# Kernel optimization log

Hardware: AMD Instinct MI355X
Metric: run time of the kernel (lower is better)

The kernel has to match this reference:

```python
import jax, jax.numpy as jnp
import numpy as np

B, T, S, C, F = 32, 50, 2048, 8, 32  # batch, time, spatial steps, in-channels, filters
K, STRIDE = 2, 2
DN = ('NWC', 'WIO', 'NWC')


def hard_sigmoid(x):
    # TF-Keras hard_sigmoid: clip(0.2*x + 0.5, 0, 1)
    return jnp.clip(0.2 * x + 0.5, 0.0, 1.0)


def setup_inputs() -> dict:
    key = jax.random.key(0)
    ks = jax.random.split(key, 5)
    x = jax.random.normal(ks[0], (B, T, S, C), jnp.float32)
    kernel = jax.random.normal(ks[1], (K, C, 4 * F), jnp.float32) * 0.05
    rec_kernel = jax.random.normal(ks[2], (K, F, 4 * F), jnp.float32) * 0.05
    bias = jnp.zeros((4 * F,), jnp.float32)
    dense_w = jax.random.normal(ks[3], ((S // STRIDE) * F, 1), jnp.float32) * 0.02
    dense_b = jnp.zeros((1,), jnp.float32)
    return dict(x=x, kernel=kernel, rec_kernel=rec_kernel, bias=bias,
                dense_w=dense_w, dense_b=dense_b)


def reference(x, kernel, rec_kernel, bias, dense_w, dense_b):
    b, t, s, c = x.shape
    f = rec_kernel.shape[1]
    # Input convolution for all timesteps at once (stride 2, SAME padding)
    xc = jax.lax.conv_general_dilated(x.reshape(b * t, s, c), kernel,
                                      (STRIDE,), 'SAME', dimension_numbers=DN)
    xc = xc + bias
    sh = xc.shape[1]  # ceil(s / stride)
    xc = xc.reshape(b, t, sh, 4 * f).transpose(1, 0, 2, 3)  # time-major for scan

    def step(carry, xt):
        h, cst = carry
        hc = jax.lax.conv_general_dilated(h, rec_kernel, (1,), 'SAME',
                                          dimension_numbers=DN)
        z = xt + hc
        zi, zf, zc, zo = jnp.split(z, 4, axis=-1)
        i = hard_sigmoid(zi)
        fg = hard_sigmoid(zf)
        cst = fg * cst + i * jnp.tanh(zc)
        o = hard_sigmoid(zo)
        h = o * jnp.tanh(cst)
        return (h, cst), None

    h0 = jnp.zeros((b, sh, f), x.dtype)
    (h, _), _ = jax.lax.scan(step, (h0, h0), xc)
    # Flatten + Dense(1)
    return h.reshape(b, -1) @ dense_w + dense_b
```

## Files before the change

kernel.cpp:

```cpp
#include <hip/hip_runtime.h>


#define TT 50
#define LTILE 64
#define ROWS 129
#define HSTR 40

typedef __attribute__((ext_vector_type(8))) short short8;
typedef __attribute__((ext_vector_type(4))) float floatx4;

__device__ short8 g_tw0[512];
__device__ short8 g_tw1[512];
__device__ short8 g_txw[512];

__device__ __forceinline__ unsigned short f2b_rne(float f) {
  union { float f; unsigned u; } v; v.f = f;
  unsigned r = v.u + 0x7FFFu + ((v.u >> 16) & 1u);
  return (unsigned short)(r >> 16);
}
__device__ __forceinline__ unsigned short f2b_trunc(float f) {
  union { float f; unsigned u; } v; v.f = f;
  return (unsigned short)(v.u >> 16);
}
__device__ __forceinline__ float hsig(float x) {
  return __builtin_amdgcn_fmed3f(__builtin_fmaf(0.2f, x, 0.5f), 0.0f, 1.0f);
}
__device__ __forceinline__ float ftanh(float x) {
  float e = __expf(2.0f * x);
  return 1.0f - 2.0f * __builtin_amdgcn_rcpf(e + 1.0f);
}

__global__ void prep(const float* __restrict__ ks,
                     const float* __restrict__ rks,
                     const float* __restrict__ bs,
                     float* __restrict__ ws) {
  const int lane = threadIdx.x;
  if (lane < 32) ws[lane] = 0.0f;
  const int q  = lane >> 4;
  const int f0 = lane & 15;
#pragma unroll
  for (int n = 0; n < 8; ++n) {
    const int oc = (n >> 1) * 32 + 2 * f0 + (n & 1);
    short8 th;
#pragma unroll
    for (int j = 0; j < 8; ++j)
      th[j] = (short)f2b_rne(rks[(q * 8 + j) * 128 + oc]);
    g_tw0[n * 64 + lane] = th;
#pragma unroll
    for (int j = 0; j < 8; ++j)
      th[j] = (short)f2b_rne(rks[(32 + q * 8 + j) * 128 + oc]);
    g_tw1[n * 64 + lane] = th;
    short8 tx = {0, 0, 0, 0, 0, 0, 0, 0};
    if (q < 2) {
#pragma unroll
      for (int j = 0; j < 8; ++j)
        tx[j] = (short)f2b_rne(ks[(q * 8 + j) * 128 + oc]);
    } else if (q == 2) {
      tx[0] = (short)f2b_rne(bs[oc]);
    }
    g_txw[n * 64 + lane] = tx;
  }
}

__global__ __launch_bounds__(256, 2)
void convlstm_scan(const float* __restrict__ xs,
                   const float* __restrict__ dws,
                   float* __restrict__ acc_out) {
  __shared__ short hbH[2][ROWS * HSTR];

  const int tid  = threadIdx.x;
  const int b    = blockIdx.x >> 4;
  const int j0   = (blockIdx.x & 15) * LTILE;
  const int wave = tid >> 6;
  const int lane = tid & 63;
  const int q    = lane >> 4;
  const int f0   = lane & 15;

  for (int e = tid; e < ROWS * HSTR; e += 256)
    ((int*)hbH)[e] = 0;

  short8 Bwh0[8], Bwh1[8], Bxw[8];
#pragma unroll
  for (int n = 0; n < 8; ++n) {
    Bwh0[n] = g_tw0[n * 64 + lane];
    Bwh1[n] = g_tw1[n * 64 + lane];
    Bxw[n]  = g_txw[n * 64 + lane];
  }

  short8 axc = {0, 0, 0, 0, 0, 0, 0, 0};
  if (q == 2) axc[0] = (short)0x3F80;

  const floatx4 zero4 = {0.0f, 0.0f, 0.0f, 0.0f};

  float cst[2][8];
#pragma unroll
  for (int s = 0; s < 2; ++s)
#pragma unroll
    for (int i = 0; i < 8; ++i) cst[s][i] = 0.0f;

  floatx4 px0[2], px1[2];
#pragma unroll
  for (int s = 0; s < 2; ++s) {
    const int jr = (wave + 4 * s) * 16 + f0;
    const int jm = min(j0 + jr, 1023);
    const float* xp = xs + (size_t)b * TT * (2048 * 8) +
                      (size_t)(2 * jm + (q & 1)) * 8;
    px0[s] = *(const floatx4*)xp;
    px1[s] = *(const floatx4*)(xp + 4);
  }

  const int maxrows = 1024 - j0;
  float part = 0.0f;
  __syncthreads();

  for (int t = 0; t < TT; ++t) {
    const short* curH = hbH[t & 1];
    short* nxtH = hbH[(t & 1) ^ 1];
    int rows = LTILE + (TT - 1) - t;
    if (rows > maxrows) rows = maxrows;
    const int nmt = (rows + 15) >> 4;
    const int act1 = (wave + 4) < nmt;
    const int last = (t == TT - 1);
    const int tn = last ? t : t + 1;
    const float* xnext = xs + ((size_t)(b * TT + tn)) * (2048 * 8);

    short8 a0h[2], a1h[2];
#pragma unroll
    for (int s = 0; s < 2; ++s) {
      const int jr = (wave + 4 * s) * 16 + f0;
      a0h[s] = *(const short8*)&curH[jr * HSTR + q * 8];
      a1h[s] = *(const short8*)&curH[(jr + 1) * HSTR + q * 8];
    }

    short8 ax[2];
#pragma unroll
    for (int s = 0; s < 2; ++s) {
      ax[s] = axc;
      if (q < 2) {
        floatx4 x0 = px0[s], x1 = px1[s];
#pragma unroll
        for (int jj = 0; jj < 4; ++jj) ax[s][jj] = (short)f2b_trunc(x0[jj]);
#pragma unroll
        for (int jj = 0; jj < 4; ++jj) ax[s][4 + jj] = (short)f2b_trunc(x1[jj]);
      }
    }

#pragma unroll
    for (int s = 0; s < 2; ++s) {
      const int jr = (wave + 4 * s) * 16 + f0;
      const int jm = min(j0 + jr, 1023);
      const float* xp = xnext + (size_t)(2 * jm + (q & 1)) * 8;
      px0[s] = *(const floatx4*)xp;
      px1[s] = *(const floatx4*)(xp + 4);
    }

#pragma unroll
    for (int s = 0; s < 2; ++s) {
      if (s == 1 && !act1) continue;
      const int m = wave + 4 * s;

      floatx4 acc[8];
#pragma unroll
      for (int n = 0; n < 8; ++n)
        acc[n] = __builtin_amdgcn_mfma_f32_16x16x32_bf16(ax[s], Bxw[n], zero4, 0, 0, 0);
#pragma unroll
      for (int n = 0; n < 8; ++n)
        acc[n] = __builtin_amdgcn_mfma_f32_16x16x32_bf16(a0h[s], Bwh0[n], acc[n], 0, 0, 0);
#pragma unroll
      for (int n = 0; n < 8; ++n)
        acc[n] = __builtin_amdgcn_mfma_f32_16x16x32_bf16(a1h[s], Bwh1[n], acc[n], 0, 0, 0);

      const int jw = m * 16 + q * 4;
#pragma unroll
      for (int r = 0; r < 4; ++r) {
        float hv2[2];
#pragma unroll
        for (int p = 0; p < 2; ++p) {
          float zi = acc[0 + p][r], zf = acc[2 + p][r];
          float zc = acc[4 + p][r], zo = acc[6 + p][r];
          float ig = hsig(zi), fg = hsig(zf), og = hsig(zo);
          float cs = cst[s][p * 4 + r];
          float cn = __builtin_fmaf(fg, cs, ig * ftanh(zc));
          cst[s][p * 4 + r] = cn;
          hv2[p] = og * ftanh(cn);
        }
        if (!last) {
          unsigned pk;
          asm("v_cvt_pk_bf16_f32 %0, %1, %2"
              : "=v"(pk) : "v"(hv2[0]), "v"(hv2[1]));
          *(unsigned*)&nxtH[(jw + r) * HSTR + 2 * f0] = pk;
        } else {
          const int di = (j0 + jw + r) * 32 + 2 * f0;
          part = __builtin_fmaf(hv2[0], dws[di],
                 __builtin_fmaf(hv2[1], dws[di + 1], part));
        }
      }
    }
    __syncthreads();
  }

#pragma unroll
  for (int off = 32; off > 0; off >>= 1) part += __shfl_down(part, off);
  if (lane == 0) atomicAdd(&acc_out[b], part);
}

__global__ void finalize(const float* __restrict__ ws,
                         const float* __restrict__ db,
                         float* __restrict__ out) {
  int i = threadIdx.x;
  if (i < 32) out[i] = ws[i] + db[0];
}

extern "C" void kernel_launch(void* const* d_in, const int* in_sizes, int n_in,
                              void* d_out, int out_size, void* d_ws, size_t ws_size,
                              hipStream_t stream) {
  const float* x  = (const float*)d_in[0];
  const float* k  = (const float*)d_in[1];
  const float* rk = (const float*)d_in[2];
  const float* bi = (const float*)d_in[3];
  const float* dw = (const float*)d_in[4];
  const float* db = (const float*)d_in[5];
  float* ws = (float*)d_ws;
  float* out = (float*)d_out;

  hipLaunchKernelGGL(prep, dim3(1), dim3(64), 0, stream, k, rk, bi, ws);
  hipLaunchKernelGGL(convlstm_scan, dim3(512), dim3(256), 0, stream,
                     x, dw, ws);
  hipLaunchKernelGGL(finalize, dim3(1), dim3(64), 0, stream, ws, db, out);
}
```

Measured before the change: 233.4 us.

## Assign one M-tile per wave with 512-thread blocks and skip idle waves

The scan kernel doubles its block to 8 waves, so each wave owns a single 16-row tile instead of looping over two. The per-wave cell state and x-prefetch registers shrink, and waves whose tile falls outside the shrinking active row range skip all work for that step. The partial-sum atomic is limited to the first four waves, since only they hold rows at the final step. The launch bound of (512, 4) caps registers per thread tightly. With about 96 VGPRs already used for resident bf16 weight fragments, this risks spills, and each block-wide barrier now spans more waves.

```diff
diff --git a/kernel.cpp b/kernel.cpp
--- a/kernel.cpp
+++ b/kernel.cpp
@@ -62,7 +62,7 @@
   }
 }
 
-__global__ __launch_bounds__(256, 2)
+__global__ __launch_bounds__(512, 4)
 void convlstm_scan(const float* __restrict__ xs,
                    const float* __restrict__ dws,
                    float* __restrict__ acc_out) {
@@ -76,7 +76,7 @@
   const int q    = lane >> 4;
   const int f0   = lane & 15;
 
-  for (int e = tid; e < ROWS * HSTR; e += 256)
+  for (int e = tid; e < ROWS * HSTR; e += 512)
     ((int*)hbH)[e] = 0;
 
   short8 Bwh0[8], Bwh1[8], Bxw[8];
@@ -92,21 +92,18 @@
 
   const floatx4 zero4 = {0.0f, 0.0f, 0.0f, 0.0f};
 
-  float cst[2][8];
-#pragma unroll
-  for (int s = 0; s < 2; ++s)
-#pragma unroll
-    for (int i = 0; i < 8; ++i) cst[s][i] = 0.0f;
-
-  floatx4 px0[2], px1[2];
-#pragma unroll
-  for (int s = 0; s < 2; ++s) {
-    const int jr = (wave + 4 * s) * 16 + f0;
-    const int jm = min(j0 + jr, 1023);
-    const float* xp = xs + (size_t)b * TT * (2048 * 8) +
-                      (size_t)(2 * jm + (q & 1)) * 8;
-    px0[s] = *(const floatx4*)xp;
-    px1[s] = *(const floatx4*)(xp + 4);
+  float cst[8];
+#pragma unroll
+  for (int i = 0; i < 8; ++i) cst[i] = 0.0f;
+
+  const int jr = wave * 16 + f0;
+  const int jm = min(j0 + jr, 1023);
+  const float* xbase = xs + (size_t)b * TT * (2048 * 8);
+  floatx4 px0 = zero4, px1 = zero4;
+  if (q < 2) {
+    const float* xp = xbase + (size_t)(2 * jm + q) * 8;
+    px0 = *(const floatx4*)xp;
+    px1 = *(const floatx4*)(xp + 4);
   }
 
   const int maxrows = 1024 - j0;
@@ -119,58 +116,39 @@
     int rows = LTILE + (TT - 1) - t;
     if (rows > maxrows) rows = maxrows;
     const int nmt = (rows + 15) >> 4;
-    const int act1 = (wave + 4) < nmt;
     const int last = (t == TT - 1);
-    const int tn = last ? t : t + 1;
-    const float* xnext = xs + ((size_t)(b * TT + tn)) * (2048 * 8);
-
-    short8 a0h[2], a1h[2];
-#pragma unroll
-    for (int s = 0; s < 2; ++s) {
-      const int jr = (wave + 4 * s) * 16 + f0;
-      a0h[s] = *(const short8*)&curH[jr * HSTR + q * 8];
-      a1h[s] = *(const short8*)&curH[(jr + 1) * HSTR + q * 8];
-    }
-
-    short8 ax[2];
-#pragma unroll
-    for (int s = 0; s < 2; ++s) {
-      ax[s] = axc;
+
+    if (wave < nmt) {
+      short8 a0h = *(const short8*)&curH[jr * HSTR + q * 8];
+      short8 a1h = *(const short8*)&curH[(jr + 1) * HSTR + q * 8];
+
+      short8 ax = axc;
       if (q < 2) {
-        floatx4 x0 = px0[s], x1 = px1[s];
-#pragma unroll
-        for (int jj = 0; jj < 4; ++jj) ax[s][jj] = (short)f2b_trunc(x0[jj]);
-#pragma unroll
-        for (int jj = 0; jj < 4; ++jj) ax[s][4 + jj] = (short)f2b_trunc(x1[jj]);
+#pragma unroll
+        for (int jj = 0; jj < 4; ++jj) ax[jj] = (short)f2b_trunc(px0[jj]);
+#pragma unroll
+        for (int jj = 0; jj < 4; ++jj) ax[4 + jj] = (short)f2b_trunc(px1[jj]);
       }
-    }
-
-#pragma unroll
-    for (int s = 0; s < 2; ++s) {
-      const int jr = (wave + 4 * s) * 16 + f0;
-      const int jm = min(j0 + jr, 1023);
-      const float* xp = xnext + (size_t)(2 * jm + (q & 1)) * 8;
-      px0[s] = *(const floatx4*)xp;
-      px1[s] = *(const floatx4*)(xp + 4);
-    }
-
-#pragma unroll
-    for (int s = 0; s < 2; ++s) {
-      if (s == 1 && !act1) continue;
-      const int m = wave + 4 * s;
+
+      const int tn = last ? t : t + 1;
+      if (q < 2) {
+        const float* xp = xbase + ((size_t)tn * 2048 + (size_t)(2 * jm + q)) * 8;
+        px0 = *(const floatx4*)xp;
+        px1 = *(const floatx4*)(xp + 4);
+      }
 
       floatx4 acc[8];
 #pragma unroll
       for (int n = 0; n < 8; ++n)
-        acc[n] = __builtin_amdgcn_mfma_f32_16x16x32_bf16(ax[s], Bxw[n], zero4, 0, 0, 0);
+        acc[n] = __builtin_amdgcn_mfma_f32_16x16x32_bf16(ax, Bxw[n], zero4, 0, 0, 0);
 #pragma unroll
       for (int n = 0; n < 8; ++n)
-        acc[n] = __builtin_amdgcn_mfma_f32_16x16x32_bf16(a0h[s], Bwh0[n], acc[n], 0, 0, 0);
+        acc[n] = __builtin_amdgcn_mfma_f32_16x16x32_bf16(a0h, Bwh0[n], acc[n], 0, 0, 0);
 #pragma unroll
       for (int n = 0; n < 8; ++n)
-        acc[n] = __builtin_amdgcn_mfma_f32_16x16x32_bf16(a1h[s], Bwh1[n], acc[n], 0, 0, 0);
-
-      const int jw = m * 16 + q * 4;
+        acc[n] = __builtin_amdgcn_mfma_f32_16x16x32_bf16(a1h, Bwh1[n], acc[n], 0, 0, 0);
+
+      const int jw = wave * 16 + q * 4;
 #pragma unroll
       for (int r = 0; r < 4; ++r) {
         float hv2[2];
@@ -179,9 +157,9 @@
           float zi = acc[0 + p][r], zf = acc[2 + p][r];
           float zc = acc[4 + p][r], zo = acc[6 + p][r];
           float ig = hsig(zi), fg = hsig(zf), og = hsig(zo);
-          float cs = cst[s][p * 4 + r];
+          float cs = cst[p * 4 + r];
           float cn = __builtin_fmaf(fg, cs, ig * ftanh(zc));
-          cst[s][p * 4 + r] = cn;
+          cst[p * 4 + r] = cn;
           hv2[p] = og * ftanh(cn);
         }
         if (!last) {
@@ -201,7 +179,7 @@
 
 #pragma unroll
   for (int off = 32; off > 0; off >>= 1) part += __shfl_down(part, off);
-  if (lane == 0) atomicAdd(&acc_out[b], part);
+  if (lane == 0 && wave < 4) atomicAdd(&acc_out[b], part);
 }
 
 __global__ void finalize(const float* __restrict__ ws,
@@ -224,7 +202,7 @@
   float* out = (float*)d_out;
 
   hipLaunchKernelGGL(prep, dim3(1), dim3(64), 0, stream, k, rk, bi, ws);
-  hipLaunchKernelGGL(convlstm_scan, dim3(512), dim3(256), 0, stream,
+  hipLaunchKernelGGL(convlstm_scan, dim3(512), dim3(512), 0, stream,
                      x, dw, ws);
   hipLaunchKernelGGL(finalize, dim3(1), dim3(64), 0, stream, ws, db, out);
 }
```

Result: slower. 355.0 us (+52.1%).

## Stage MFMA weight fragments in LDS and raise occupancy to three blocks

Applied to the files above, without the earlier changes.

Moves the three sets of bf16 weight fragments out of per-thread registers into shared memory. Each MFMA now reads its B operand from LDS inside the timestep loop, and the launch bound rises to three blocks per CU to exploit the freed VGPRs. Input prefetch is also restricted to the lanes that use it (q<2), which removes redundant global loads. The cost is roughly 24 KB of extra LDS reads per wave per timestep and higher LDS pressure. More resident blocks are meant to hide the latency of the serial scan.

```diff
diff --git a/kernel.cpp b/kernel.cpp
--- a/kernel.cpp
+++ b/kernel.cpp
@@ -62,11 +62,14 @@
   }
 }
 
-__global__ __launch_bounds__(256, 2)
+__global__ __launch_bounds__(256, 3)
 void convlstm_scan(const float* __restrict__ xs,
                    const float* __restrict__ dws,
                    float* __restrict__ acc_out) {
   __shared__ short hbH[2][ROWS * HSTR];
+  __shared__ short8 sTw0[512];
+  __shared__ short8 sTw1[512];
+  __shared__ short8 sTxw[512];
 
   const int tid  = threadIdx.x;
   const int b    = blockIdx.x >> 4;
@@ -78,13 +81,10 @@
 
   for (int e = tid; e < ROWS * HSTR; e += 256)
     ((int*)hbH)[e] = 0;
-
-  short8 Bwh0[8], Bwh1[8], Bxw[8];
-#pragma unroll
-  for (int n = 0; n < 8; ++n) {
-    Bwh0[n] = g_tw0[n * 64 + lane];
-    Bwh1[n] = g_tw1[n * 64 + lane];
-    Bxw[n]  = g_txw[n * 64 + lane];
+  for (int e = tid; e < 512; e += 256) {
+    sTw0[e] = g_tw0[e];
+    sTw1[e] = g_tw1[e];
+    sTxw[e] = g_txw[e];
   }
 
   short8 axc = {0, 0, 0, 0, 0, 0, 0, 0};
@@ -101,12 +101,15 @@
   floatx4 px0[2], px1[2];
 #pragma unroll
   for (int s = 0; s < 2; ++s) {
+    px0[s] = zero4; px1[s] = zero4;
     const int jr = (wave + 4 * s) * 16 + f0;
     const int jm = min(j0 + jr, 1023);
-    const float* xp = xs + (size_t)b * TT * (2048 * 8) +
-                      (size_t)(2 * jm + (q & 1)) * 8;
-    px0[s] = *(const floatx4*)xp;
-    px1[s] = *(const floatx4*)(xp + 4);
+    if (q < 2) {
+      const float* xp = xs + (size_t)b * TT * (2048 * 8) +
+                        (size_t)(2 * jm + q) * 8;
+      px0[s] = *(const floatx4*)xp;
+      px1[s] = *(const floatx4*)(xp + 4);
+    }
   }
 
   const int maxrows = 1024 - j0;
@@ -149,9 +152,11 @@
     for (int s = 0; s < 2; ++s) {
       const int jr = (wave + 4 * s) * 16 + f0;
       const int jm = min(j0 + jr, 1023);
-      const float* xp = xnext + (size_t)(2 * jm + (q & 1)) * 8;
-      px0[s] = *(const floatx4*)xp;
-      px1[s] = *(const floatx4*)(xp + 4);
+      if (q < 2) {
+        const float* xp = xnext + (size_t)(2 * jm + q) * 8;
+        px0[s] = *(const floatx4*)xp;
+        px1[s] = *(const floatx4*)(xp + 4);
+      }
     }
 
 #pragma unroll
@@ -161,14 +166,20 @@
 
       floatx4 acc[8];
 #pragma unroll
-      for (int n = 0; n < 8; ++n)
-        acc[n] = __builtin_amdgcn_mfma_f32_16x16x32_bf16(ax[s], Bxw[n], zero4, 0, 0, 0);
-#pragma unroll
-      for (int n = 0; n < 8; ++n)
-        acc[n] = __builtin_amdgcn_mfma_f32_16x16x32_bf16(a0h[s], Bwh0[n], acc[n], 0, 0, 0);
-#pragma unroll
-      for (int n = 0; n < 8; ++n)
-        acc[n] = __builtin_amdgcn_mfma_f32_16x16x32_bf16(a1h[s], Bwh1[n], acc[n], 0, 0, 0);
+      for (int n = 0; n < 8; ++n) {
+        short8 bx = sTxw[n * 64 + lane];
+        acc[n] = __builtin_amdgcn_mfma_f32_16x16x32_bf16(ax[s], bx, zero4, 0, 0, 0);
+      }
+#pragma unroll
+      for (int n = 0; n < 8; ++n) {
+        short8 bw = sTw0[n * 64 + lane];
+        acc[n] = __builtin_amdgcn_mfma_f32_16x16x32_bf16(a0h[s], bw, acc[n], 0, 0, 0);
+      }
+#pragma unroll
+      for (int n = 0; n < 8; ++n) {
+        short8 bw = sTw1[n * 64 + lane];
+        acc[n] = __builtin_amdgcn_mfma_f32_16x16x32_bf16(a1h[s], bw, acc[n], 0, 0, 0);
+      }
 
       const int jw = m * 16 + q * 4;
 #pragma unroll
```

New measurement: 244.2 us. 4.6% more time.

## Halve recompute halo by exchanging mid-scan boundary state between neighbor tiles

Applied to the files above, without the earlier changes.

Each block used to recompute a halo of 49 extra rows so that it could run all 50 timesteps independently. Now the halo covers only 25 steps. At t=25 each block publishes its h and c boundary state to global memory and raises a flag, and its neighbor spins on that flag and loads the state to extend its tile for the remaining steps. Blocks are assigned in reverse tile order so that producers are scheduled first. Smaller changes also parallelize prep over 512 threads and skip unneeded x loads and inactive LDS reads. The inter-block spin-wait cuts redundant MFMA work, but it depends on co-residency and forward progress and adds a global-memory synchronization point.

```diff
diff --git a/kernel.cpp b/kernel.cpp
--- a/kernel.cpp
+++ b/kernel.cpp
@@ -2,8 +2,9 @@
 
 
 #define TT 50
+#define HD 25
 #define LTILE 64
-#define ROWS 129
+#define ROWS 97
 #define HSTR 40
 
 typedef __attribute__((ext_vector_type(8))) short short8;
@@ -12,6 +13,10 @@
 __device__ short8 g_tw0[512];
 __device__ short8 g_tw1[512];
 __device__ short8 g_txw[512];
+
+__device__ unsigned g_xh[512 * 400];
+__device__ float    g_xc[512 * 800];
+__device__ int      g_flag[512];
 
 __device__ __forceinline__ unsigned short f2b_rne(float f) {
   union { float f; unsigned u; } v; v.f = f;
@@ -34,32 +39,33 @@
                      const float* __restrict__ rks,
                      const float* __restrict__ bs,
                      float* __restrict__ ws) {
-  const int lane = threadIdx.x;
-  if (lane < 32) ws[lane] = 0.0f;
-  const int q  = lane >> 4;
-  const int f0 = lane & 15;
-#pragma unroll
-  for (int n = 0; n < 8; ++n) {
-    const int oc = (n >> 1) * 32 + 2 * f0 + (n & 1);
-    short8 th;
+  const int tid  = threadIdx.x;
+  const int n    = tid >> 6;
+  const int lane = tid & 63;
+  const int q    = lane >> 4;
+  const int f0   = lane & 15;
+  if (tid < 32) ws[tid] = 0.0f;
+  g_flag[tid] = 0;
+
+  const int oc = (n >> 1) * 32 + 2 * f0 + (n & 1);
+  short8 th;
+#pragma unroll
+  for (int j = 0; j < 8; ++j)
+    th[j] = (short)f2b_rne(rks[(q * 8 + j) * 128 + oc]);
+  g_tw0[n * 64 + lane] = th;
+#pragma unroll
+  for (int j = 0; j < 8; ++j)
+    th[j] = (short)f2b_rne(rks[(32 + q * 8 + j) * 128 + oc]);
+  g_tw1[n * 64 + lane] = th;
+  short8 tx = {0, 0, 0, 0, 0, 0, 0, 0};
+  if (q < 2) {
 #pragma unroll
     for (int j = 0; j < 8; ++j)
-      th[j] = (short)f2b_rne(rks[(q * 8 + j) * 128 + oc]);
-    g_tw0[n * 64 + lane] = th;
-#pragma unroll
-    for (int j = 0; j < 8; ++j)
-      th[j] = (short)f2b_rne(rks[(32 + q * 8 + j) * 128 + oc]);
-    g_tw1[n * 64 + lane] = th;
-    short8 tx = {0, 0, 0, 0, 0, 0, 0, 0};
-    if (q < 2) {
-#pragma unroll
-      for (int j = 0; j < 8; ++j)
-        tx[j] = (short)f2b_rne(ks[(q * 8 + j) * 128 + oc]);
-    } else if (q == 2) {
-      tx[0] = (short)f2b_rne(bs[oc]);
-    }
-    g_txw[n * 64 + lane] = tx;
+      tx[j] = (short)f2b_rne(ks[(q * 8 + j) * 128 + oc]);
+  } else if (q == 2) {
+    tx[0] = (short)f2b_rne(bs[oc]);
   }
+  g_txw[n * 64 + lane] = tx;
 }
 
 __global__ __launch_bounds__(256, 2)
@@ -70,11 +76,15 @@
 
   const int tid  = threadIdx.x;
   const int b    = blockIdx.x >> 4;
-  const int j0   = (blockIdx.x & 15) * LTILE;
+  const int pi   = blockIdx.x & 15;
+  const int tj   = 15 - pi;
+  const int j0   = tj << 6;
   const int wave = tid >> 6;
   const int lane = tid & 63;
   const int q    = lane >> 4;
   const int f0   = lane & 15;
+  const bool is_pub = (pi < 15);
+  const bool is_con = (pi >= 1);
 
   for (int e = tid; e < ROWS * HSTR; e += 256)
     ((int*)hbH)[e] = 0;
@@ -89,7 +99,6 @@
 
   short8 axc = {0, 0, 0, 0, 0, 0, 0, 0};
   if (q == 2) axc[0] = (short)0x3F80;
-
   const floatx4 zero4 = {0.0f, 0.0f, 0.0f, 0.0f};
 
   float cst[2][8];
@@ -101,12 +110,15 @@
   floatx4 px0[2], px1[2];
 #pragma unroll
   for (int s = 0; s < 2; ++s) {
+    px0[s] = zero4; px1[s] = zero4;
     const int jr = (wave + 4 * s) * 16 + f0;
     const int jm = min(j0 + jr, 1023);
-    const float* xp = xs + (size_t)b * TT * (2048 * 8) +
-                      (size_t)(2 * jm + (q & 1)) * 8;
-    px0[s] = *(const floatx4*)xp;
-    px1[s] = *(const floatx4*)(xp + 4);
+    if (q < 2) {
+      const float* xp = xs + (size_t)b * TT * (2048 * 8) +
+                        (size_t)(2 * jm + q) * 8;
+      px0[s] = *(const floatx4*)xp;
+      px1[s] = *(const floatx4*)(xp + 4);
+    }
   }
 
   const int maxrows = 1024 - j0;
@@ -114,9 +126,69 @@
   __syncthreads();
 
   for (int t = 0; t < TT; ++t) {
+    if (t == HD) {
+      short* bufH = hbH[HD & 1];
+      if (is_pub) {
+        for (int e = tid; e < 400; e += 256) {
+          const int row = e >> 4, d = e & 15;
+          g_xh[blockIdx.x * 400 + e] = *(const unsigned*)&bufH[row * HSTR + 2 * d];
+        }
+        if (wave == 0) {
+#pragma unroll
+          for (int r = 0; r < 4; ++r)
+#pragma unroll
+            for (int pp = 0; pp < 2; ++pp)
+              g_xc[blockIdx.x * 800 + (q * 4 + r) * 32 + 2 * f0 + pp] = cst[0][pp * 4 + r];
+        } else if (wave == 1) {
+#pragma unroll
+          for (int r = 0; r < 4; ++r)
+            if (q * 4 + r <= 8) {
+#pragma unroll
+              for (int pp = 0; pp < 2; ++pp)
+                g_xc[blockIdx.x * 800 + (16 + q * 4 + r) * 32 + 2 * f0 + pp] = cst[0][pp * 4 + r];
+            }
+        }
+      }
+      __threadfence();
+      __syncthreads();
+      if (is_pub && tid == 0)
+        __hip_atomic_store(&g_flag[blockIdx.x], 1, __ATOMIC_RELEASE,
+                           __HIP_MEMORY_SCOPE_AGENT);
+      if (is_con) {
+        if (tid == 0) {
+          while (__hip_atomic_load(&g_flag[blockIdx.x - 1], __ATOMIC_RELAXED,
+                                   __HIP_MEMORY_SCOPE_AGENT) == 0)
+            __builtin_amdgcn_s_sleep(2);
+        }
+        __syncthreads();
+        __builtin_amdgcn_fence(__ATOMIC_ACQUIRE, "agent");
+        for (int e = tid; e < 400; e += 256) {
+          const int row = e >> 4, d = e & 15;
+          *(unsigned*)&bufH[(64 + row) * HSTR + 2 * d] =
+              g_xh[(blockIdx.x - 1) * 400 + e];
+        }
+        if (wave == 0) {
+#pragma unroll
+          for (int r = 0; r < 4; ++r)
+#pragma unroll
+            for (int pp = 0; pp < 2; ++pp)
+              cst[1][pp * 4 + r] = g_xc[(blockIdx.x - 1) * 800 + (q * 4 + r) * 32 + 2 * f0 + pp];
+        } else if (wave == 1) {
+#pragma unroll
+          for (int r = 0; r < 4; ++r)
+            if (q * 4 + r <= 8) {
+#pragma unroll
+              for (int pp = 0; pp < 2; ++pp)
+                cst[1][pp * 4 + r] = g_xc[(blockIdx.x - 1) * 800 + (16 + q * 4 + r) * 32 + 2 * f0 + pp];
+            }
+        }
+      }
+      __syncthreads();
+    }
+
     const short* curH = hbH[t & 1];
     short* nxtH = hbH[(t & 1) ^ 1];
-    int rows = LTILE + (TT - 1) - t;
+    int rows = LTILE - 1 + ((t < HD) ? HD : TT) - t;
     if (rows > maxrows) rows = maxrows;
     const int nmt = (rows + 15) >> 4;
     const int act1 = (wave + 4) < nmt;
@@ -127,6 +199,7 @@
     short8 a0h[2], a1h[2];
 #pragma unroll
     for (int s = 0; s < 2; ++s) {
+      if (s == 1 && !act1) continue;
       const int jr = (wave + 4 * s) * 16 + f0;
       a0h[s] = *(const short8*)&curH[jr * HSTR + q * 8];
       a1h[s] = *(const short8*)&curH[(jr + 1) * HSTR + q * 8];
@@ -147,9 +220,10 @@
 
 #pragma unroll
     for (int s = 0; s < 2; ++s) {
+      if (q >= 2) continue;
       const int jr = (wave + 4 * s) * 16 + f0;
       const int jm = min(j0 + jr, 1023);
-      const float* xp = xnext + (size_t)(2 * jm + (q & 1)) * 8;
+      const float* xp = xnext + (size_t)(2 * jm + q) * 8;
       px0[s] = *(const floatx4*)xp;
       px1[s] = *(const floatx4*)(xp + 4);
     }
@@ -223,7 +297,7 @@
   float* ws = (float*)d_ws;
   float* out = (float*)d_out;
 
-  hipLaunchKernelGGL(prep, dim3(1), dim3(64), 0, stream, k, rk, bi, ws);
+  hipLaunchKernelGGL(prep, dim3(1), dim3(512), 0, stream, k, rk, bi, ws);
   hipLaunchKernelGGL(convlstm_scan, dim3(512), dim3(256), 0, stream,
                      x, dw, ws);
   hipLaunchKernelGGL(finalize, dim3(1), dim3(64), 0, stream, ws, db, out);
```

Measured after the change: 334.8 us. 43.4% more time.
